# Kernel optimization log

Hardware: AMD Instinct MI355X
Metric: run time of the kernel (lower is better)

Reference implementation:

```python
import jax, jax.numpy as jnp
import numpy as np

H, I, E, K = 1024, 2816, 8, 2  # hidden, intermediate, n_experts, topk
B, S = 2, 2048


def setup_inputs() -> dict:
    key = jax.random.key(0)
    ks = jax.random.split(key, 6)
    def init(k, shape, fan_in):
        return (jax.random.normal(k, shape, jnp.float32) / np.sqrt(fan_in)).astype(jnp.float32)
    return {
        "x": jax.random.normal(ks[0], (B, S, H), jnp.float32),
        "Wgate": init(ks[1], (H, E), H),   # gating Linear weight (in,out layout)
        "bgate": jnp.zeros((E,), jnp.float32),  # gating Linear bias (nn.Linear default bias=True)
        "Wg": init(ks[2], (E, H, I), H),   # stacked gate_proj, mlp_bias=False
        "Wu": init(ks[3], (E, H, I), H),   # stacked up_proj
        "Wd": init(ks[4], (E, I, H), I),   # stacked down_proj
    }


def reference(x, Wgate, bgate, Wg, Wu, Wd):
    Bb, Ss, Hd = x.shape
    xf = x.reshape(-1, Hd)                       # [N, H] flattened tokens
    logits = xf @ Wgate + bgate                  # [N, E] gate logits
    topv, topi = jax.lax.top_k(logits, K)        # [N, K]
    N = xf.shape[0]
    # sparse combine weights: raw top-k LOGITS (no softmax), zeros elsewhere
    # (faithful to torch: scatter of logits_topk into -inf mask; -inf slots
    #  are never read since only selected experts contribute)
    combine = jnp.zeros_like(logits).at[jnp.arange(N)[:, None], topi].set(topv)  # [N, E]
    # dense grouped SwiGLU over all experts, then sparse combine
    g = jnp.einsum('nh,ehi->nei', xf, Wg)        # [N, E, I]
    u = jnp.einsum('nh,ehi->nei', xf, Wu)        # [N, E, I]
    h = jax.nn.silu(g) * u                       # [N, E, I]
    eo = jnp.einsum('nei,eih->neh', h, Wd)       # [N, E, H]
    out = jnp.einsum('neh,ne->nh', eo, combine).reshape(Bb, Ss, Hd)
    return out, logits
```

## Files before the change

### kernel.cpp

```cpp
#include <hip/hip_runtime.h>

#define HDIM 1024
#define IDIM 2816
#define NEXP 8
#define NTOK 4096
#define NROWS 8192
#define RPAD 8320
#define MT   64
#define GU_NY 22
#define DN_NY 8

typedef short bf16x8 __attribute__((ext_vector_type(8)));
typedef float f32x4 __attribute__((ext_vector_type(4)));
typedef unsigned short u16x8 __attribute__((ext_vector_type(8)));

static __device__ __forceinline__ float bf2f(unsigned int u) {
    union { unsigned int i; float f; } v; v.i = u << 16; return v.f;
}
static __device__ __forceinline__ unsigned short f2bf(float f) {
    union { float f; unsigned int i; } v; v.f = f;
    return (unsigned short)((v.i + 0x7fffu + ((v.i >> 16) & 1u)) >> 16);
}

static __device__ __forceinline__ void gload16(const void* g, void* l) {
    __builtin_amdgcn_global_load_lds(
        (const __attribute__((address_space(1))) unsigned int*)g,
        (__attribute__((address_space(3))) unsigned int*)l, 16, 0, 0);
}

__global__ __launch_bounds__(256) void gating_kernel(
    const float* __restrict__ x, const float* __restrict__ Wgate,
    const float* __restrict__ bgate, float* __restrict__ logits_out,
    int* __restrict__ counts, int* __restrict__ topi, float* __restrict__ topv)
{
    int wave = (blockIdx.x << 2) + (threadIdx.x >> 6);
    int lane = threadIdx.x & 63;
    if (wave >= NTOK) return;
    const float* xr = x + (size_t)wave * HDIM;

    double acc[NEXP];
#pragma unroll
    for (int e = 0; e < NEXP; ++e) acc[e] = 0.0;

    for (int it = 0; it < HDIM / 64; ++it) {
        int h = lane + (it << 6);
        float xv = xr[h];
        const float* wr = Wgate + (size_t)h * NEXP;
#pragma unroll
        for (int e = 0; e < NEXP; ++e) acc[e] += (double)xv * (double)wr[e];
    }
#pragma unroll
    for (int e = 0; e < NEXP; ++e) {
        double v = acc[e];
        for (int off = 32; off; off >>= 1) v += __shfl_xor(v, off, 64);
        acc[e] = v + (double)bgate[e];
    }
    float lf[NEXP];
#pragma unroll
    for (int e = 0; e < NEXP; ++e) lf[e] = (float)acc[e];

    if (lane < NEXP) logits_out[(size_t)wave * NEXP + lane] = lf[lane];

    if (lane == 0) {
        int i1 = 0; float v1 = lf[0];
#pragma unroll
        for (int e = 1; e < NEXP; ++e) if (lf[e] > v1) { v1 = lf[e]; i1 = e; }
        int i2 = -1; float v2 = -3.0e38f;
#pragma unroll
        for (int e = 0; e < NEXP; ++e) {
            if (e == i1) continue;
            if (lf[e] > v2) { v2 = lf[e]; i2 = e; }
        }
        topi[wave * 2 + 0] = i1; topv[wave * 2 + 0] = v1;
        topi[wave * 2 + 1] = i2; topv[wave * 2 + 1] = v2;
        atomicAdd(&counts[i1], 1);
        atomicAdd(&counts[i2], 1);
    }
}

__global__ void offsets_kernel(const int* __restrict__ counts,
                               int* __restrict__ offs, int* __restrict__ cursor)
{
    if (threadIdx.x == 0 && blockIdx.x == 0) {
        int s = 0;
        for (int e = 0; e < NEXP; ++e) { offs[e] = s; cursor[e] = s; s += counts[e]; }
        offs[NEXP] = s;
    }
}

__global__ __launch_bounds__(256) void scatter_kernel(
    const float* __restrict__ x, const int* __restrict__ topi,
    const float* __restrict__ topv, int* __restrict__ cursor,
    float* __restrict__ row_w, int* __restrict__ pos_of,
    unsigned short* __restrict__ Xg)
{
    int p = (blockIdx.x << 2) + (threadIdx.x >> 6);
    int lane = threadIdx.x & 63;
    if (p >= NROWS) return;
    int n = p >> 1;
    int e = topi[p];
    float w = topv[p];
    int pos = 0;
    if (lane == 0) {
        pos = atomicAdd(&cursor[e], 1);
        row_w[pos] = w;
        pos_of[p] = pos;
    }
    pos = __shfl(pos, 0, 64);
    const float* xr = x + (size_t)n * HDIM;
    unsigned short* dst = Xg + (size_t)pos * HDIM;
#pragma unroll
    for (int it = 0; it < HDIM / 256; ++it) {
        int idx = (it * 64 + lane) * 4;
        float4 v = *reinterpret_cast<const float4*>(&xr[idx]);
        ushort4 o;
        o.x = f2bf(v.x); o.y = f2bf(v.y); o.z = f2bf(v.z); o.w = f2bf(v.w);
        *reinterpret_cast<ushort4*>(&dst[idx]) = o;
    }
}

__global__ __launch_bounds__(256) void transpose_cvt_kernel(
    const float* __restrict__ src, unsigned short* __restrict__ dst,
    int R, int C, int TC)
{
    __shared__ unsigned short lds[64 * 66];
    int e = blockIdx.y;
    const float* s0 = src + (size_t)e * R * C;
    unsigned short* d0 = dst + (size_t)e * R * C;
    int tt = blockIdx.x;
    int tr = tt / TC, tc = tt % TC;
    int tid = threadIdx.x;
    {
        int r = tid >> 2, c0 = (tid & 3) << 4;
        const float* s = s0 + (size_t)(tr * 64 + r) * C + tc * 64 + c0;
        float4 v0 = *reinterpret_cast<const float4*>(s);
        float4 v1 = *reinterpret_cast<const float4*>(s + 4);
        float4 v2 = *reinterpret_cast<const float4*>(s + 8);
        float4 v3 = *reinterpret_cast<const float4*>(s + 12);
        unsigned short* lr_ = &lds[r * 66 + c0];
        lr_[0]  = f2bf(v0.x); lr_[1]  = f2bf(v0.y); lr_[2]  = f2bf(v0.z); lr_[3]  = f2bf(v0.w);
        lr_[4]  = f2bf(v1.x); lr_[5]  = f2bf(v1.y); lr_[6]  = f2bf(v1.z); lr_[7]  = f2bf(v1.w);
        lr_[8]  = f2bf(v2.x); lr_[9]  = f2bf(v2.y); lr_[10] = f2bf(v2.z); lr_[11] = f2bf(v2.w);
        lr_[12] = f2bf(v3.x); lr_[13] = f2bf(v3.y); lr_[14] = f2bf(v3.z); lr_[15] = f2bf(v3.w);
    }
    __syncthreads();
    {
        int c = tid >> 2, q0 = (tid & 3) << 4;
        u16x8 o0, o1;
#pragma unroll
        for (int j = 0; j < 8; ++j) o0[j] = lds[(q0 + j) * 66 + c];
#pragma unroll
        for (int j = 0; j < 8; ++j) o1[j] = lds[(q0 + 8 + j) * 66 + c];
        unsigned short* d = d0 + (size_t)(tc * 64 + c) * R + tr * 64 + q0;
        *reinterpret_cast<u16x8*>(d) = o0;
        *reinterpret_cast<u16x8*>(d + 8) = o1;
    }
}

__global__ __launch_bounds__(256, 2) void gateup_kernel(
    const unsigned short* __restrict__ Xg,
    const unsigned short* __restrict__ Wgt,
    const unsigned short* __restrict__ Wut,
    const int* __restrict__ offs, unsigned short* __restrict__ hbuf)
{
    __shared__ unsigned short As[128 * 64];
    __shared__ unsigned short Bgs[128 * 64];
    __shared__ unsigned short Bus[128 * 64];

    int bid = blockIdx.x;
    int slot = bid >> 3, xcd = bid & 7;
    int L = xcd * (NEXP * GU_NY * MT / 8) + slot;
    int mt = L & (MT - 1);
    int t = L >> 6;
    int ny = t % GU_NY;
    int e  = t / GU_NY;

    const int r0 = offs[e], r1 = offs[e + 1];
    const int m0 = r0 + mt * 128;
    if (m0 >= r1) return;
    const int n0 = ny * 128;

    const unsigned short* wg = Wgt + (size_t)e * IDIM * HDIM;
    const unsigned short* wu = Wut + (size_t)e * IDIM * HDIM;

    const int tid = threadIdx.x;
    const int lane = tid & 63, wv = tid >> 6;
    const int wr = (wv >> 1) * 64, wc = (wv & 1) * 64;
    const int lr = lane & 15, kg = (lane >> 4) * 8;
    const int srow = lane >> 3;
    const int scol = (lane & 7) * 8;

    f32x4 zero = {0.f, 0.f, 0.f, 0.f};
    f32x4 accg[4][4], accu[4][4];
#pragma unroll
    for (int m = 0; m < 4; ++m)
#pragma unroll
        for (int n = 0; n < 4; ++n) { accg[m][n] = zero; accu[m][n] = zero; }

    for (int k0 = 0; k0 < HDIM; k0 += 64) {
        __syncthreads();
#pragma unroll
        for (int i = 0; i < 4; ++i) {
            int chunk = i * 4 + wv;
            int row = chunk * 8 + srow;
            unsigned short* la = &As[chunk * 512 + lane * 8];
            unsigned short* lg = &Bgs[chunk * 512 + lane * 8];
            unsigned short* lu = &Bus[chunk * 512 + lane * 8];
            gload16(&Xg[(size_t)(m0 + row) * HDIM + k0 + scol], la);
            gload16(&wg[(size_t)(n0 + row) * HDIM + k0 + scol], lg);
            gload16(&wu[(size_t)(n0 + row) * HDIM + k0 + scol], lu);
        }
        __syncthreads();

#pragma unroll
        for (int ks = 0; ks < 2; ++ks) {
            bf16x8 af[4], bg[4], bu[4];
#pragma unroll
            for (int m = 0; m < 4; ++m)
                af[m] = *reinterpret_cast<const bf16x8*>(&As[(wr + m * 16 + lr) * 64 + ks * 32 + kg]);
#pragma unroll
            for (int n = 0; n < 4; ++n) {
                bg[n] = *reinterpret_cast<const bf16x8*>(&Bgs[(wc + n * 16 + lr) * 64 + ks * 32 + kg]);
                bu[n] = *reinterpret_cast<const bf16x8*>(&Bus[(wc + n * 16 + lr) * 64 + ks * 32 + kg]);
            }
#pragma unroll
            for (int m = 0; m < 4; ++m)
#pragma unroll
                for (int n = 0; n < 4; ++n) {
                    accg[m][n] = __builtin_amdgcn_mfma_f32_16x16x32_bf16(af[m], bg[n], accg[m][n], 0, 0, 0);
                    accu[m][n] = __builtin_amdgcn_mfma_f32_16x16x32_bf16(af[m], bu[n], accu[m][n], 0, 0, 0);
                }
        }
    }

    const int rr = (lane >> 4) * 4;
#pragma unroll
    for (int m = 0; m < 4; ++m) {
#pragma unroll
        for (int r = 0; r < 4; ++r) {
            int grow = m0 + wr + m * 16 + rr + r;
            if (grow < r1) {
                unsigned short* hr = &hbuf[(size_t)grow * IDIM + n0 + wc + lr];
#pragma unroll
                for (int n = 0; n < 4; ++n) {
                    float g = accg[m][n][r];
                    float u = accu[m][n][r];
                    float s = g / (1.0f + __expf(-g));
                    hr[n * 16] = f2bf(s * u);
                }
            }
        }
    }
}

__global__ __launch_bounds__(256, 2) void down_kernel(
    const unsigned short* __restrict__ hbuf,
    const unsigned short* __restrict__ Wdt,
    const int* __restrict__ offs,
    const float* __restrict__ row_w,
    unsigned short* __restrict__ eo)
{
    __shared__ unsigned short As[128 * 64];
    __shared__ unsigned short Bs[128 * 64];

    int bid = blockIdx.x;
    int slot = bid >> 3, xcd = bid & 7;
    int L = xcd * (NEXP * DN_NY * MT / 8) + slot;
    int mt = L & (MT - 1);
    int t = L >> 6;
    int ny = t & (DN_NY - 1);
    int e  = t >> 3;

    const int r0 = offs[e], r1 = offs[e + 1];
    const int m0 = r0 + mt * 128;
    if (m0 >= r1) return;
    const int n0 = ny * 128;

    const unsigned short* wd = Wdt + (size_t)e * HDIM * IDIM;

    const int tid = threadIdx.x;
    const int lane = tid & 63, wv = tid >> 6;
    const int wr = (wv >> 1) * 64, wc = (wv & 1) * 64;
    const int lr = lane & 15, kg = (lane >> 4) * 8;
    const int srow = lane >> 3;
    const int scol = (lane & 7) * 8;

    f32x4 zero = {0.f, 0.f, 0.f, 0.f};
    f32x4 acc[4][4];
#pragma unroll
    for (int m = 0; m < 4; ++m)
#pragma unroll
        for (int n = 0; n < 4; ++n) acc[m][n] = zero;

    for (int k0 = 0; k0 < IDIM; k0 += 64) {
        __syncthreads();
#pragma unroll
        for (int i = 0; i < 4; ++i) {
            int chunk = i * 4 + wv;
            int row = chunk * 8 + srow;
            unsigned short* la = &As[chunk * 512 + lane * 8];
            unsigned short* lb = &Bs[chunk * 512 + lane * 8];
            gload16(&hbuf[(size_t)(m0 + row) * IDIM + k0 + scol], la);
            gload16(&wd[(size_t)(n0 + row) * IDIM + k0 + scol], lb);
        }
        __syncthreads();

#pragma unroll
        for (int ks = 0; ks < 2; ++ks) {
            bf16x8 af[4], bf[4];
#pragma unroll
            for (int m = 0; m < 4; ++m)
                af[m] = *reinterpret_cast<const bf16x8*>(&As[(wr + m * 16 + lr) * 64 + ks * 32 + kg]);
#pragma unroll
            for (int n = 0; n < 4; ++n)
                bf[n] = *reinterpret_cast<const bf16x8*>(&Bs[(wc + n * 16 + lr) * 64 + ks * 32 + kg]);
#pragma unroll
            for (int m = 0; m < 4; ++m)
#pragma unroll
                for (int n = 0; n < 4; ++n)
                    acc[m][n] = __builtin_amdgcn_mfma_f32_16x16x32_bf16(af[m], bf[n], acc[m][n], 0, 0, 0);
        }
    }

    const int rr = (lane >> 4) * 4;
#pragma unroll
    for (int m = 0; m < 4; ++m) {
#pragma unroll
        for (int r = 0; r < 4; ++r) {
            int grow = m0 + wr + m * 16 + rr + r;
            if (grow < r1) {
                float w = row_w[grow];
                unsigned short* er = &eo[(size_t)grow * HDIM + n0 + wc + lr];
#pragma unroll
                for (int n = 0; n < 4; ++n)
                    er[n * 16] = f2bf(acc[m][n][r] * w);
            }
        }
    }
}

__global__ __launch_bounds__(256) void combine_kernel(
    const unsigned short* __restrict__ eo, const int* __restrict__ pos_of,
    float* __restrict__ out)
{
    int t = blockIdx.x * 256 + threadIdx.x;
    int n = t >> 7;
    int c = (t & 127) << 3;
    int p0 = pos_of[n * 2 + 0];
    int p1 = pos_of[n * 2 + 1];
    uint4 a = *reinterpret_cast<const uint4*>(&eo[(size_t)p0 * HDIM + c]);
    uint4 b = *reinterpret_cast<const uint4*>(&eo[(size_t)p1 * HDIM + c]);
    float4 o0, o1;
    o0.x = bf2f(a.x & 0xffffu) + bf2f(b.x & 0xffffu);
    o0.y = bf2f(a.x >> 16)     + bf2f(b.x >> 16);
    o0.z = bf2f(a.y & 0xffffu) + bf2f(b.y & 0xffffu);
    o0.w = bf2f(a.y >> 16)     + bf2f(b.y >> 16);
    o1.x = bf2f(a.z & 0xffffu) + bf2f(b.z & 0xffffu);
    o1.y = bf2f(a.z >> 16)     + bf2f(b.z >> 16);
    o1.z = bf2f(a.w & 0xffffu) + bf2f(b.w & 0xffffu);
    o1.w = bf2f(a.w >> 16)     + bf2f(b.w >> 16);
    float* op = out + (size_t)n * HDIM + c;
    *reinterpret_cast<float4*>(op) = o0;
    *reinterpret_cast<float4*>(op + 4) = o1;
}

extern "C" void kernel_launch(void* const* d_in, const int* in_sizes, int n_in,
                              void* d_out, int out_size, void* d_ws, size_t ws_size,
                              hipStream_t stream)
{
    const float* x     = (const float*)d_in[0];
    const float* Wgate = (const float*)d_in[1];
    const float* bgate = (const float*)d_in[2];
    const float* Wg    = (const float*)d_in[3];
    const float* Wu    = (const float*)d_in[4];
    const float* Wd    = (const float*)d_in[5];
    float* out = (float*)d_out;
    float* logits = out + (size_t)NTOK * HDIM;

    char* ws = (char*)d_ws;
    unsigned short* Xg   = (unsigned short*)ws;
    unsigned short* hbuf = (unsigned short*)(ws + 17039360);
    unsigned short* Wgt  = (unsigned short*)(ws + 63897600);
    unsigned short* Wut  = (unsigned short*)(ws + 110034944);
    char* meta = ws + 156172288;
    int*   counts = (int*)(meta);
    int*   offs   = (int*)(meta + 64);
    int*   cursor = (int*)(meta + 128);
    int*   topi   = (int*)(meta + 256);
    float* topv   = (float*)(meta + 33024);
    int*   pos_of = (int*)(meta + 65792);
    float* row_w  = (float*)(meta + 98560);

    hipMemsetAsync(counts, 0, 32, stream);
    gating_kernel<<<NTOK / 4, 256, 0, stream>>>(x, Wgate, bgate, logits, counts, topi, topv);
    offsets_kernel<<<1, 64, 0, stream>>>(counts, offs, cursor);
    scatter_kernel<<<NROWS / 4, 256, 0, stream>>>(x, topi, topv, cursor, row_w, pos_of, Xg);

    transpose_cvt_kernel<<<dim3(704, NEXP), 256, 0, stream>>>(Wg, Wgt, HDIM, IDIM, IDIM / 64);
    transpose_cvt_kernel<<<dim3(704, NEXP), 256, 0, stream>>>(Wu, Wut, HDIM, IDIM, IDIM / 64);

    gateup_kernel<<<NEXP * GU_NY * MT, 256, 0, stream>>>(Xg, Wgt, Wut, offs, hbuf);

    transpose_cvt_kernel<<<dim3(704, NEXP), 256, 0, stream>>>(Wd, Wgt, IDIM, HDIM, HDIM / 64);

    down_kernel<<<NEXP * DN_NY * MT, 256, 0, stream>>>(hbuf, Wgt, offs, row_w, Xg );
    combine_kernel<<<NTOK * HDIM / 8 / 256, 256, 0, stream>>>(Xg, pos_of, out);
}
```

Before: 560.8 us.

## Compact MoE tile list, interleave gate/up weights, atomic combine in down GEMM

Builds a compact list of (expert, row-tile) pairs so the GEMM grids launch only real tiles instead of a padded 64-tile-per-expert grid full of early-exit blocks. Gate and up weights are interleaved into one buffer in 16-row groups, so a single accumulator set holds both projections and the SwiGLU pairs are taken from adjacent tiles. This halves the LDS footprint and registers, and occupancy is raised to 4. The down kernel now atomically adds weighted results straight into a zeroed fp32 output, which removes the expert-output buffer and the combine kernel. The cost is an extra memset of the output and atomic contention.

```diff
diff --git a/kernel.cpp b/kernel.cpp
--- a/kernel.cpp
+++ b/kernel.cpp
@@ -6,17 +6,16 @@
 #define NTOK 4096
 #define NROWS 8192
 #define RPAD 8320
-#define MT   64
-#define GU_NY 22
-#define DN_NY 8
+#define MAXT 71
+#define GU_NYT 44
+#define DN_NYT 8
+#define GU_NWG (MAXT * GU_NYT)
+#define DN_NWG (MAXT * DN_NYT)
 
 typedef short bf16x8 __attribute__((ext_vector_type(8)));
 typedef float f32x4 __attribute__((ext_vector_type(4)));
 typedef unsigned short u16x8 __attribute__((ext_vector_type(8)));
 
-static __device__ __forceinline__ float bf2f(unsigned int u) {
-    union { unsigned int i; float f; } v; v.i = u << 16; return v.f;
-}
 static __device__ __forceinline__ unsigned short f2bf(float f) {
     union { float f; unsigned int i; } v; v.f = f;
     return (unsigned short)((v.i + 0x7fffu + ((v.i >> 16) & 1u)) >> 16);
@@ -79,19 +78,27 @@
 }
 
 __global__ void offsets_kernel(const int* __restrict__ counts,
-                               int* __restrict__ offs, int* __restrict__ cursor)
+                               int* __restrict__ offs, int* __restrict__ cursor,
+                               int* __restrict__ ntile, int* __restrict__ te,
+                               int* __restrict__ tm0)
 {
     if (threadIdx.x == 0 && blockIdx.x == 0) {
         int s = 0;
         for (int e = 0; e < NEXP; ++e) { offs[e] = s; cursor[e] = s; s += counts[e]; }
         offs[NEXP] = s;
+        int nt = 0;
+        for (int e = 0; e < NEXP; ++e) {
+            int c = counts[e], base = offs[e];
+            for (int mt = 0; mt * 128 < c; ++mt) { te[nt] = e; tm0[nt] = base + mt * 128; ++nt; }
+        }
+        *ntile = nt;
     }
 }
 
 __global__ __launch_bounds__(256) void scatter_kernel(
     const float* __restrict__ x, const int* __restrict__ topi,
     const float* __restrict__ topv, int* __restrict__ cursor,
-    float* __restrict__ row_w, int* __restrict__ pos_of,
+    float* __restrict__ row_w, int* __restrict__ tok_of,
     unsigned short* __restrict__ Xg)
 {
     int p = (blockIdx.x << 2) + (threadIdx.x >> 6);
@@ -104,7 +111,7 @@
     if (lane == 0) {
         pos = atomicAdd(&cursor[e], 1);
         row_w[pos] = w;
-        pos_of[p] = pos;
+        tok_of[pos] = n;
     }
     pos = __shfl(pos, 0, 64);
     const float* xr = x + (size_t)n * HDIM;
@@ -119,20 +126,22 @@
     }
 }
 
-__global__ __launch_bounds__(256) void transpose_cvt_kernel(
-    const float* __restrict__ src, unsigned short* __restrict__ dst,
-    int R, int C, int TC)
+__global__ __launch_bounds__(256) void transpose_cvt_gu_kernel(
+    const float* __restrict__ Wg, const float* __restrict__ Wu,
+    unsigned short* __restrict__ W2)
 {
     __shared__ unsigned short lds[64 * 66];
-    int e = blockIdx.y;
-    const float* s0 = src + (size_t)e * R * C;
-    unsigned short* d0 = dst + (size_t)e * R * C;
+    const int kind = blockIdx.z;
+    const int e = blockIdx.y;
+    const float* s0 = (kind ? Wu : Wg) + (size_t)e * HDIM * IDIM;
+    unsigned short* d0 = W2 + (size_t)e * 2 * IDIM * HDIM;
+    const int TC = IDIM / 64;
     int tt = blockIdx.x;
     int tr = tt / TC, tc = tt % TC;
     int tid = threadIdx.x;
     {
         int r = tid >> 2, c0 = (tid & 3) << 4;
-        const float* s = s0 + (size_t)(tr * 64 + r) * C + tc * 64 + c0;
+        const float* s = s0 + (size_t)(tr * 64 + r) * IDIM + tc * 64 + c0;
         float4 v0 = *reinterpret_cast<const float4*>(s);
         float4 v1 = *reinterpret_cast<const float4*>(s + 4);
         float4 v2 = *reinterpret_cast<const float4*>(s + 8);
@@ -151,37 +160,76 @@
         for (int j = 0; j < 8; ++j) o0[j] = lds[(q0 + j) * 66 + c];
 #pragma unroll
         for (int j = 0; j < 8; ++j) o1[j] = lds[(q0 + 8 + j) * 66 + c];
-        unsigned short* d = d0 + (size_t)(tc * 64 + c) * R + tr * 64 + q0;
+        int i = tc * 64 + c;
+        int r2 = ((i >> 4) << 5) + (kind << 4) + (i & 15);
+        unsigned short* d = d0 + (size_t)r2 * HDIM + tr * 64 + q0;
         *reinterpret_cast<u16x8*>(d) = o0;
         *reinterpret_cast<u16x8*>(d + 8) = o1;
     }
 }
 
-__global__ __launch_bounds__(256, 2) void gateup_kernel(
+__global__ __launch_bounds__(256) void transpose_cvt_d_kernel(
+    const float* __restrict__ Wd, unsigned short* __restrict__ Wdt)
+{
+    __shared__ unsigned short lds[64 * 66];
+    const int e = blockIdx.y;
+    const float* s0 = Wd + (size_t)e * IDIM * HDIM;
+    unsigned short* d0 = Wdt + (size_t)e * HDIM * IDIM;
+    const int TC = HDIM / 64;
+    int tt = blockIdx.x;
+    int tr = tt / TC, tc = tt % TC;
+    int tid = threadIdx.x;
+    {
+        int r = tid >> 2, c0 = (tid & 3) << 4;
+        const float* s = s0 + (size_t)(tr * 64 + r) * HDIM + tc * 64 + c0;
+        float4 v0 = *reinterpret_cast<const float4*>(s);
+        float4 v1 = *reinterpret_cast<const float4*>(s + 4);
+        float4 v2 = *reinterpret_cast<const float4*>(s + 8);
+        float4 v3 = *reinterpret_cast<const float4*>(s + 12);
+        unsigned short* lr_ = &lds[r * 66 + c0];
+        lr_[0]  = f2bf(v0.x); lr_[1]  = f2bf(v0.y); lr_[2]  = f2bf(v0.z); lr_[3]  = f2bf(v0.w);
+        lr_[4]  = f2bf(v1.x); lr_[5]  = f2bf(v1.y); lr_[6]  = f2bf(v1.z); lr_[7]  = f2bf(v1.w);
+        lr_[8]  = f2bf(v2.x); lr_[9]  = f2bf(v2.y); lr_[10] = f2bf(v2.z); lr_[11] = f2bf(v2.w);
+        lr_[12] = f2bf(v3.x); lr_[13] = f2bf(v3.y); lr_[14] = f2bf(v3.z); lr_[15] = f2bf(v3.w);
+    }
+    __syncthreads();
+    {
+        int c = tid >> 2, q0 = (tid & 3) << 4;
+        u16x8 o0, o1;
+#pragma unroll
+        for (int j = 0; j < 8; ++j) o0[j] = lds[(q0 + j) * 66 + c];
+#pragma unroll
+        for (int j = 0; j < 8; ++j) o1[j] = lds[(q0 + 8 + j) * 66 + c];
+        unsigned short* d = d0 + (size_t)(tc * 64 + c) * IDIM + tr * 64 + q0;
+        *reinterpret_cast<u16x8*>(d) = o0;
+        *reinterpret_cast<u16x8*>(d + 8) = o1;
+    }
+}
+
+__global__ __launch_bounds__(256, 4) void gateup_kernel(
     const unsigned short* __restrict__ Xg,
-    const unsigned short* __restrict__ Wgt,
-    const unsigned short* __restrict__ Wut,
-    const int* __restrict__ offs, unsigned short* __restrict__ hbuf)
+    const unsigned short* __restrict__ W2,
+    const int* __restrict__ offs,
+    const int* __restrict__ ntile, const int* __restrict__ te,
+    const int* __restrict__ tm0, unsigned short* __restrict__ hbuf)
 {
     __shared__ unsigned short As[128 * 64];
-    __shared__ unsigned short Bgs[128 * 64];
-    __shared__ unsigned short Bus[128 * 64];
+    __shared__ unsigned short Bs[128 * 64];
 
     int bid = blockIdx.x;
-    int slot = bid >> 3, xcd = bid & 7;
-    int L = xcd * (NEXP * GU_NY * MT / 8) + slot;
-    int mt = L & (MT - 1);
-    int t = L >> 6;
-    int ny = t % GU_NY;
-    int e  = t / GU_NY;
-
-    const int r0 = offs[e], r1 = offs[e + 1];
-    const int m0 = r0 + mt * 128;
-    if (m0 >= r1) return;
+    int xcd = bid & 7, rest = bid >> 3;
+    const int q = GU_NWG / 8, r = GU_NWG % 8;
+    int wg = (xcd < r ? xcd * (q + 1) : r * (q + 1) + (xcd - r) * q) + rest;
+    int t = wg % MAXT;
+    int ny = wg / MAXT;
+
+    if (t >= *ntile) return;
+    const int e = te[t];
+    const int m0 = tm0[t];
+    const int r1 = offs[e + 1];
     const int n0 = ny * 128;
 
-    const unsigned short* wg = Wgt + (size_t)e * IDIM * HDIM;
-    const unsigned short* wu = Wut + (size_t)e * IDIM * HDIM;
+    const unsigned short* wb = W2 + (size_t)e * 2 * IDIM * HDIM;
 
     const int tid = threadIdx.x;
     const int lane = tid & 63, wv = tid >> 6;
@@ -191,11 +239,11 @@
     const int scol = (lane & 7) * 8;
 
     f32x4 zero = {0.f, 0.f, 0.f, 0.f};
-    f32x4 accg[4][4], accu[4][4];
+    f32x4 acc[4][4];
 #pragma unroll
     for (int m = 0; m < 4; ++m)
 #pragma unroll
-        for (int n = 0; n < 4; ++n) { accg[m][n] = zero; accu[m][n] = zero; }
+        for (int n = 0; n < 4; ++n) acc[m][n] = zero;
 
     for (int k0 = 0; k0 < HDIM; k0 += 64) {
         __syncthreads();
@@ -203,77 +251,69 @@
         for (int i = 0; i < 4; ++i) {
             int chunk = i * 4 + wv;
             int row = chunk * 8 + srow;
-            unsigned short* la = &As[chunk * 512 + lane * 8];
-            unsigned short* lg = &Bgs[chunk * 512 + lane * 8];
-            unsigned short* lu = &Bus[chunk * 512 + lane * 8];
-            gload16(&Xg[(size_t)(m0 + row) * HDIM + k0 + scol], la);
-            gload16(&wg[(size_t)(n0 + row) * HDIM + k0 + scol], lg);
-            gload16(&wu[(size_t)(n0 + row) * HDIM + k0 + scol], lu);
+            gload16(&Xg[(size_t)(m0 + row) * HDIM + k0 + scol], &As[chunk * 512 + lane * 8]);
+            gload16(&wb[(size_t)(n0 + row) * HDIM + k0 + scol], &Bs[chunk * 512 + lane * 8]);
         }
         __syncthreads();
 
 #pragma unroll
         for (int ks = 0; ks < 2; ++ks) {
-            bf16x8 af[4], bg[4], bu[4];
+            bf16x8 af[4], bf[4];
 #pragma unroll
             for (int m = 0; m < 4; ++m)
                 af[m] = *reinterpret_cast<const bf16x8*>(&As[(wr + m * 16 + lr) * 64 + ks * 32 + kg]);
 #pragma unroll
-            for (int n = 0; n < 4; ++n) {
-                bg[n] = *reinterpret_cast<const bf16x8*>(&Bgs[(wc + n * 16 + lr) * 64 + ks * 32 + kg]);
-                bu[n] = *reinterpret_cast<const bf16x8*>(&Bus[(wc + n * 16 + lr) * 64 + ks * 32 + kg]);
+            for (int n = 0; n < 4; ++n)
+                bf[n] = *reinterpret_cast<const bf16x8*>(&Bs[(wc + n * 16 + lr) * 64 + ks * 32 + kg]);
+#pragma unroll
+            for (int m = 0; m < 4; ++m)
+#pragma unroll
+                for (int n = 0; n < 4; ++n)
+                    acc[m][n] = __builtin_amdgcn_mfma_f32_16x16x32_bf16(af[m], bf[n], acc[m][n], 0, 0, 0);
+        }
+    }
+
+    const int rr = (lane >> 4) * 4;
+    const int iloc0 = ((wc >> 5) << 4) + lr;
+    const int col0 = ny * 64 + iloc0;
+#pragma unroll
+    for (int m = 0; m < 4; ++m) {
+#pragma unroll
+        for (int j = 0; j < 4; ++j) {
+            int grow = m0 + wr + m * 16 + rr + j;
+            if (grow < r1) {
+                unsigned short* hr = &hbuf[(size_t)grow * IDIM + col0];
+                float g0 = acc[m][0][j], u0 = acc[m][1][j];
+                float g1 = acc[m][2][j], u1 = acc[m][3][j];
+                hr[0]  = f2bf(g0 / (1.0f + __expf(-g0)) * u0);
+                hr[16] = f2bf(g1 / (1.0f + __expf(-g1)) * u1);
             }
-#pragma unroll
-            for (int m = 0; m < 4; ++m)
-#pragma unroll
-                for (int n = 0; n < 4; ++n) {
-                    accg[m][n] = __builtin_amdgcn_mfma_f32_16x16x32_bf16(af[m], bg[n], accg[m][n], 0, 0, 0);
-                    accu[m][n] = __builtin_amdgcn_mfma_f32_16x16x32_bf16(af[m], bu[n], accu[m][n], 0, 0, 0);
-                }
-        }
-    }
-
-    const int rr = (lane >> 4) * 4;
-#pragma unroll
-    for (int m = 0; m < 4; ++m) {
-#pragma unroll
-        for (int r = 0; r < 4; ++r) {
-            int grow = m0 + wr + m * 16 + rr + r;
-            if (grow < r1) {
-                unsigned short* hr = &hbuf[(size_t)grow * IDIM + n0 + wc + lr];
-#pragma unroll
-                for (int n = 0; n < 4; ++n) {
-                    float g = accg[m][n][r];
-                    float u = accu[m][n][r];
-                    float s = g / (1.0f + __expf(-g));
-                    hr[n * 16] = f2bf(s * u);
-                }
-            }
-        }
-    }
-}
-
-__global__ __launch_bounds__(256, 2) void down_kernel(
+        }
+    }
+}
+
+__global__ __launch_bounds__(256, 4) void down_kernel(
     const unsigned short* __restrict__ hbuf,
     const unsigned short* __restrict__ Wdt,
     const int* __restrict__ offs,
-    const float* __restrict__ row_w,
-    unsigned short* __restrict__ eo)
+    const int* __restrict__ ntile, const int* __restrict__ te,
+    const int* __restrict__ tm0,
+    const float* __restrict__ row_w, const int* __restrict__ tok_of,
+    float* __restrict__ out)
 {
     __shared__ unsigned short As[128 * 64];
     __shared__ unsigned short Bs[128 * 64];
 
     int bid = blockIdx.x;
-    int slot = bid >> 3, xcd = bid & 7;
-    int L = xcd * (NEXP * DN_NY * MT / 8) + slot;
-    int mt = L & (MT - 1);
-    int t = L >> 6;
-    int ny = t & (DN_NY - 1);
-    int e  = t >> 3;
-
-    const int r0 = offs[e], r1 = offs[e + 1];
-    const int m0 = r0 + mt * 128;
-    if (m0 >= r1) return;
+    int xcd = bid & 7, rest = bid >> 3;
+    int wg = xcd * (DN_NWG / 8) + rest;
+    int t = wg % MAXT;
+    int ny = wg / MAXT;
+
+    if (t >= *ntile) return;
+    const int e = te[t];
+    const int m0 = tm0[t];
+    const int r1 = offs[e + 1];
     const int n0 = ny * 128;
 
     const unsigned short* wd = Wdt + (size_t)e * HDIM * IDIM;
@@ -298,10 +338,8 @@
         for (int i = 0; i < 4; ++i) {
             int chunk = i * 4 + wv;
             int row = chunk * 8 + srow;
-            unsigned short* la = &As[chunk * 512 + lane * 8];
-            unsigned short* lb = &Bs[chunk * 512 + lane * 8];
-            gload16(&hbuf[(size_t)(m0 + row) * IDIM + k0 + scol], la);
-            gload16(&wd[(size_t)(n0 + row) * IDIM + k0 + scol], lb);
+            gload16(&hbuf[(size_t)(m0 + row) * IDIM + k0 + scol], &As[chunk * 512 + lane * 8]);
+            gload16(&wd[(size_t)(n0 + row) * IDIM + k0 + scol], &Bs[chunk * 512 + lane * 8]);
         }
         __syncthreads();
 
@@ -326,42 +364,18 @@
 #pragma unroll
     for (int m = 0; m < 4; ++m) {
 #pragma unroll
-        for (int r = 0; r < 4; ++r) {
-            int grow = m0 + wr + m * 16 + rr + r;
+        for (int j = 0; j < 4; ++j) {
+            int grow = m0 + wr + m * 16 + rr + j;
             if (grow < r1) {
                 float w = row_w[grow];
-                unsigned short* er = &eo[(size_t)grow * HDIM + n0 + wc + lr];
+                int tok = tok_of[grow];
+                float* orow = out + (size_t)tok * HDIM + n0 + wc + lr;
 #pragma unroll
                 for (int n = 0; n < 4; ++n)
-                    er[n * 16] = f2bf(acc[m][n][r] * w);
+                    atomicAdd(&orow[n * 16], acc[m][n][j] * w);
             }
         }
     }
-}
-
-__global__ __launch_bounds__(256) void combine_kernel(
-    const unsigned short* __restrict__ eo, const int* __restrict__ pos_of,
-    float* __restrict__ out)
-{
-    int t = blockIdx.x * 256 + threadIdx.x;
-    int n = t >> 7;
-    int c = (t & 127) << 3;
-    int p0 = pos_of[n * 2 + 0];
-    int p1 = pos_of[n * 2 + 1];
-    uint4 a = *reinterpret_cast<const uint4*>(&eo[(size_t)p0 * HDIM + c]);
-    uint4 b = *reinterpret_cast<const uint4*>(&eo[(size_t)p1 * HDIM + c]);
-    float4 o0, o1;
-    o0.x = bf2f(a.x & 0xffffu) + bf2f(b.x & 0xffffu);
-    o0.y = bf2f(a.x >> 16)     + bf2f(b.x >> 16);
-    o0.z = bf2f(a.y & 0xffffu) + bf2f(b.y & 0xffffu);
-    o0.w = bf2f(a.y >> 16)     + bf2f(b.y >> 16);
-    o1.x = bf2f(a.z & 0xffffu) + bf2f(b.z & 0xffffu);
-    o1.y = bf2f(a.z >> 16)     + bf2f(b.z >> 16);
-    o1.z = bf2f(a.w & 0xffffu) + bf2f(b.w & 0xffffu);
-    o1.w = bf2f(a.w >> 16)     + bf2f(b.w >> 16);
-    float* op = out + (size_t)n * HDIM + c;
-    *reinterpret_cast<float4*>(op) = o0;
-    *reinterpret_cast<float4*>(op + 4) = o1;
 }
 
 extern "C" void kernel_launch(void* const* d_in, const int* in_sizes, int n_in,
@@ -380,29 +394,31 @@
     char* ws = (char*)d_ws;
     unsigned short* Xg   = (unsigned short*)ws;
     unsigned short* hbuf = (unsigned short*)(ws + 17039360);
-    unsigned short* Wgt  = (unsigned short*)(ws + 63897600);
-    unsigned short* Wut  = (unsigned short*)(ws + 110034944);
+    unsigned short* W2   = (unsigned short*)(ws + 63897600);
     char* meta = ws + 156172288;
     int*   counts = (int*)(meta);
     int*   offs   = (int*)(meta + 64);
     int*   cursor = (int*)(meta + 128);
-    int*   topi   = (int*)(meta + 256);
-    float* topv   = (float*)(meta + 33024);
-    int*   pos_of = (int*)(meta + 65792);
-    float* row_w  = (float*)(meta + 98560);
+    int*   ntile  = (int*)(meta + 192);
+    int*   te     = (int*)(meta + 256);
+    int*   tm0    = (int*)(meta + 768);
+    int*   topi   = (int*)(meta + 2048);
+    float* topv   = (float*)(meta + 34816);
+    float* row_w  = (float*)(meta + 67584);
+    int*   tok_of = (int*)(meta + 100352);
 
     hipMemsetAsync(counts, 0, 32, stream);
+    hipMemsetAsync(out, 0, (size_t)NTOK * HDIM * sizeof(float), stream);
+
     gating_kernel<<<NTOK / 4, 256, 0, stream>>>(x, Wgate, bgate, logits, counts, topi, topv);
-    offsets_kernel<<<1, 64, 0, stream>>>(counts, offs, cursor);
-    scatter_kernel<<<NROWS / 4, 256, 0, stream>>>(x, topi, topv, cursor, row_w, pos_of, Xg);
-
-    transpose_cvt_kernel<<<dim3(704, NEXP), 256, 0, stream>>>(Wg, Wgt, HDIM, IDIM, IDIM / 64);
-    transpose_cvt_kernel<<<dim3(704, NEXP), 256, 0, stream>>>(Wu, Wut, HDIM, IDIM, IDIM / 64);
-
-    gateup_kernel<<<NEXP * GU_NY * MT, 256, 0, stream>>>(Xg, Wgt, Wut, offs, hbuf);
-
-    transpose_cvt_kernel<<<dim3(704, NEXP), 256, 0, stream>>>(Wd, Wgt, IDIM, HDIM, HDIM / 64);
-
-    down_kernel<<<NEXP * DN_NY * MT, 256, 0, stream>>>(hbuf, Wgt, offs, row_w, Xg );
-    combine_kernel<<<NTOK * HDIM / 8 / 256, 256, 0, stream>>>(Xg, pos_of, out);
-}
+    offsets_kernel<<<1, 64, 0, stream>>>(counts, offs, cursor, ntile, te, tm0);
+    scatter_kernel<<<NROWS / 4, 256, 0, stream>>>(x, topi, topv, cursor, row_w, tok_of, Xg);
+
+    transpose_cvt_gu_kernel<<<dim3((HDIM / 64) * (IDIM / 64), NEXP, 2), 256, 0, stream>>>(Wg, Wu, W2);
+
+    gateup_kernel<<<GU_NWG, 256, 0, stream>>>(Xg, W2, offs, ntile, te, tm0, hbuf);
+
+    transpose_cvt_d_kernel<<<dim3((IDIM / 64) * (HDIM / 64), NEXP), 256, 0, stream>>>(Wd, W2);
+
+    down_kernel<<<DN_NWG, 256, 0, stream>>>(hbuf, W2, offs, ntile, te, tm0, row_w, tok_of, out);
+}
```

Result: faster. 515.2 us (-8.1%).
